# Kernel tuning notes

Measured on AMD Instinct MI355X. Metric: run time of the kernel, lower is better.

The kernel has to match this reference:

```python
import jax, jax.numpy as jnp
import numpy as np
from functools import partial

V, BS, L, H, C = 50257, 1024, 6, 12, 768
HD = C // H

def _ln(x, w, b):
    mu = jnp.mean(x, axis=-1, keepdims=True)
    var = jnp.var(x, axis=-1, keepdims=True)
    return (x - mu) * jax.lax.rsqrt(var + 1e-5) * w + b

def setup_inputs() -> dict:
    key = jax.random.key(0)
    ks = jax.random.split(key, 12)
    s = 0.02
    inp = {
        "idx": jax.random.randint(ks[0], (4, 1024), 0, V, dtype=jnp.int32),
        "wte": jax.random.normal(ks[1], (V, C), jnp.float32) * s,
        "wpe": jax.random.normal(ks[2], (BS, C), jnp.float32) * s,
        # per-block stacked params; linear weights stored [in, out]
        "ln1_w": jnp.ones((L, C)), "ln1_b": jnp.zeros((L, C)),
        "attn_w": jax.random.normal(ks[3], (L, C, 3 * C), jnp.float32) * s,
        "attn_b": jnp.zeros((L, 3 * C)),
        "proj_w": jax.random.normal(ks[4], (L, C, C), jnp.float32) * s,
        "proj_b": jnp.zeros((L, C)),
        "ln2_w": jnp.ones((L, C)), "ln2_b": jnp.zeros((L, C)),
        "fc_w": jax.random.normal(ks[5], (L, C, 4 * C), jnp.float32) * s,
        "fc_b": jnp.zeros((L, 4 * C)),
        "fc2_w": jax.random.normal(ks[6], (L, 4 * C, C), jnp.float32) * s,
        "fc2_b": jnp.zeros((L, C)),
        "lnf_w": jnp.ones((C,)), "lnf_b": jnp.zeros((C,)),
    }
    return inp

def _forward(idx, wte, wpe, ln1_w, ln1_b, attn_w, attn_b, proj_w, proj_b,
             ln2_w, ln2_b, fc_w, fc_b, fc2_w, fc2_b, lnf_w, lnf_b):
    B, T = idx.shape
    x = wte[idx] + wpe[:T]  # [B,T,C]
    causal = jnp.tril(jnp.ones((T, T), bool))  # [T,T]
    scale = 1.0 / np.sqrt(HD)
    neg_inf = jnp.finfo(x.dtype).min

    def block(x, p):
        l1w, l1b, aw, ab, pw, pb, l2w, l2b, fw, fb, f2w, f2b = p
        h = _ln(x, l1w, l1b)
        qkv = h @ aw + ab  # [B,T,3C]
        q, k, v = jnp.split(qkv, 3, axis=-1)
        q = q.reshape(B, T, H, HD)
        k = k.reshape(B, T, H, HD)
        v = v.reshape(B, T, H, HD)
        att = jnp.einsum('bqhd,bkhd->bhqk', q, k) * scale
        att = jnp.where(causal, att, neg_inf)
        att = jax.nn.softmax(att, axis=-1)
        y = jnp.einsum('bhqk,bkhd->bqhd', att, v).reshape(B, T, C)
        x = x + y @ pw + pb
        h = _ln(x, l2w, l2b)
        h = jax.nn.gelu(h @ fw + fb, approximate=False)  # torch nn.GELU default = exact
        x = x + h @ f2w + f2b
        return x, None

    params = (ln1_w, ln1_b, attn_w, attn_b, proj_w, proj_b,
              ln2_w, ln2_b, fc_w, fc_b, fc2_w, fc2_b)
    x, _ = jax.lax.scan(block, x, params)
    x = _ln(x, lnf_w, lnf_b)
    logits = x @ wte.T  # tied lm_head, no bias
    return logits

def reference(idx, wte, wpe, ln1_w, ln1_b, attn_w, attn_b, proj_w, proj_b,
              ln2_w, ln2_b, fc_w, fc_b, fc2_w, fc2_b, lnf_w, lnf_b):
    return _forward(idx, wte, wpe, ln1_w, ln1_b, attn_w, attn_b, proj_w, proj_b,
                    ln2_w, ln2_b, fc_w, fc_b, fc2_w, fc2_b, lnf_w, lnf_b)
```

## Files before the change

kernel.cpp:

```cpp
#include <hip/hip_runtime.h>

#define BT     4096
#define CDIM   768
#define NLAYER 6
#define NHEAD  12
#define VREAL  50257
#define VPAD   50432

typedef __bf16 bf16x8 __attribute__((ext_vector_type(8)));
typedef float  f32x4  __attribute__((ext_vector_type(4)));

__device__ __forceinline__ unsigned short f2bf(float f) {
    unsigned int u = __builtin_bit_cast(unsigned int, f);
    u += 0x7fffu + ((u >> 16) & 1u);
    return (unsigned short)(u >> 16);
}

__device__ __forceinline__ void gload16(const unsigned short* g, unsigned short* l) {
    __builtin_amdgcn_global_load_lds(
        (const __attribute__((address_space(1))) unsigned int*)g,
        (__attribute__((address_space(3))) unsigned int*)l, 16, 0, 0);
}

__device__ __forceinline__ void swz_block(int &bx, int &by) {
    int gx = gridDim.x;
    int nwg = gx * gridDim.y;
    if ((nwg & 7) == 0) {
        int lin = by * gx + bx;
        int q = nwg >> 3;
        lin = (lin & 7) * q + (lin >> 3);
        bx = lin % gx;
        by = lin / gx;
    }
}

__global__ __launch_bounds__(256) void transpose_conv(
    const float* __restrict__ in, unsigned short* __restrict__ out, int K, int N)
{
    in  += (size_t)blockIdx.z * K * N;
    out += (size_t)blockIdx.z * K * N;
    __shared__ float t[32][33];
    int j0 = blockIdx.x * 32;
    int i0 = blockIdx.y * 32;
    int c = threadIdx.x;
    int r = threadIdx.y;
    #pragma unroll
    for (int rr = r; rr < 32; rr += 8)
        t[rr][c] = in[(size_t)(i0 + rr) * N + j0 + c];
    __syncthreads();
    #pragma unroll
    for (int rr = r; rr < 32; rr += 8)
        out[(size_t)(j0 + rr) * K + i0 + c] = f2bf(t[c][rr]);
}

__global__ __launch_bounds__(256) void wteconv(
    const float* __restrict__ wte, unsigned short* __restrict__ out)
{
    size_t e = ((size_t)blockIdx.x * 256 + threadIdx.x) * 4;
    int row = (int)(e / CDIM);
    int col = (int)(e % CDIM);
    ushort4 o;
    if (row < VREAL) {
        float4 v = *(const float4*)(wte + (size_t)row * CDIM + col);
        o.x = f2bf(v.x); o.y = f2bf(v.y); o.z = f2bf(v.z); o.w = f2bf(v.w);
    } else {
        o.x = 0; o.y = 0; o.z = 0; o.w = 0;
    }
    *(ushort4*)(out + e) = o;
}

__global__ __launch_bounds__(256) void embed_kernel(
    const int* __restrict__ idx, const float* __restrict__ wte,
    const float* __restrict__ wpe, float* __restrict__ x)
{
    int row = blockIdx.x;
    int t = row & 1023;
    int id = idx[row];
    const float* s = wte + (size_t)id * CDIM;
    const float* p = wpe + (size_t)t * CDIM;
    float* o = x + (size_t)row * CDIM;
    for (int c = threadIdx.x; c < CDIM; c += 256) o[c] = s[c] + p[c];
}

__global__ __launch_bounds__(256) void ln_kernel(
    const float* __restrict__ x, const float* __restrict__ w,
    const float* __restrict__ b, unsigned short* __restrict__ out)
{
    int row = blockIdx.x * 4 + (threadIdx.x >> 6);
    int lane = threadIdx.x & 63;
    const float* xp = x + (size_t)row * CDIM;
    float4 v[3];
    float s = 0.f, sq = 0.f;
    #pragma unroll
    for (int j = 0; j < 3; ++j) {
        v[j] = *(const float4*)(xp + j * 256 + lane * 4);
        s  += v[j].x + v[j].y + v[j].z + v[j].w;
        sq += v[j].x * v[j].x + v[j].y * v[j].y
            + v[j].z * v[j].z + v[j].w * v[j].w;
    }
    #pragma unroll
    for (int o = 32; o > 0; o >>= 1) {
        s  += __shfl_xor(s, o, 64);
        sq += __shfl_xor(sq, o, 64);
    }
    float mu  = s * (1.f / CDIM);
    float var = sq * (1.f / CDIM) - mu * mu;
    float rs  = rsqrtf(var + 1e-5f);
    unsigned short* op = out + (size_t)row * CDIM;
    #pragma unroll
    for (int j = 0; j < 3; ++j) {
        int c = j * 256 + lane * 4;
        float4 w4 = *(const float4*)(w + c);
        float4 b4 = *(const float4*)(b + c);
        ushort4 o4;
        o4.x = f2bf((v[j].x - mu) * rs * w4.x + b4.x);
        o4.y = f2bf((v[j].y - mu) * rs * w4.y + b4.y);
        o4.z = f2bf((v[j].z - mu) * rs * w4.z + b4.z);
        o4.w = f2bf((v[j].w - mu) * rs * w4.w + b4.w);
        *(ushort4*)(op + c) = o4;
    }
}

template<int MODE>
__global__ __launch_bounds__(256) void gemm_kernel(
    const unsigned short* __restrict__ A, const unsigned short* __restrict__ Bt,
    const float* __restrict__ bias, const float* __restrict__ resid,
    float* __restrict__ outF, unsigned short* __restrict__ outB,
    unsigned short* __restrict__ qout, unsigned short* __restrict__ kout,
    unsigned short* __restrict__ vtout,
    int K, int Nout)
{
    __shared__ alignas(16) unsigned short As[2][4096];
    __shared__ alignas(16) unsigned short Bs[2][4096];
    const int tid  = threadIdx.x;
    const int wv   = tid >> 6;
    const int lane = tid & 63;
    const int m0 = blockIdx.x * 128;
    const int n0 = blockIdx.y * 128;
    const int wr = wv >> 1, wc = wv & 1;
    const int srow = lane >> 2;
    const int skk  = (lane & 3) * 8;
    const int fr = lane & 15;
    const int fg = lane >> 4;
    const int fk = fg * 8;

    f32x4 acc[4][4];
    #pragma unroll
    for (int i = 0; i < 4; ++i)
        #pragma unroll
        for (int j = 0; j < 4; ++j) acc[i][j] = f32x4{0.f, 0.f, 0.f, 0.f};

    for (int k0 = 0; k0 < K; k0 += 64) {
        #pragma unroll
        for (int j = 0; j < 2; ++j) {
            int row = j * 64 + wv * 16 + srow;
            const unsigned short* ga = A  + (size_t)(m0 + row) * K + k0 + skk;
            const unsigned short* gb = Bt + (size_t)(n0 + row) * K + k0 + skk;
            gload16(ga,      &As[0][j * 2048 + wv * 512]);
            gload16(ga + 32, &As[1][j * 2048 + wv * 512]);
            gload16(gb,      &Bs[0][j * 2048 + wv * 512]);
            gload16(gb + 32, &Bs[1][j * 2048 + wv * 512]);
        }
        __syncthreads();
        #pragma unroll
        for (int ks = 0; ks < 2; ++ks) {
            bf16x8 a[4], bb[4];
            #pragma unroll
            for (int m = 0; m < 4; ++m)
                a[m] = *(const bf16x8*)&As[ks][(wr * 64 + m * 16 + fr) * 32 + fk];
            #pragma unroll
            for (int n = 0; n < 4; ++n)
                bb[n] = *(const bf16x8*)&Bs[ks][(wc * 64 + n * 16 + fr) * 32 + fk];
            #pragma unroll
            for (int m = 0; m < 4; ++m)
                #pragma unroll
                for (int n = 0; n < 4; ++n)
                    acc[m][n] = __builtin_amdgcn_mfma_f32_16x16x32_bf16(
                        bb[n], a[m], acc[m][n], 0, 0, 0);
        }
        __syncthreads();
    }

    #pragma unroll
    for (int m = 0; m < 4; ++m) {
        int row = m0 + wr * 64 + m * 16 + fr;
        #pragma unroll
        for (int n = 0; n < 4; ++n) {
            int col = n0 + wc * 64 + n * 16 + fg * 4;
            float4 bs = *(const float4*)&bias[col];
            float u0 = acc[m][n][0] + bs.x;
            float u1 = acc[m][n][1] + bs.y;
            float u2 = acc[m][n][2] + bs.z;
            float u3 = acc[m][n][3] + bs.w;
            if (MODE == 2) {
                ushort4 p;
                p.x = f2bf(0.5f * u0 * (1.f + erff(u0 * 0.70710678118654752f)));
                p.y = f2bf(0.5f * u1 * (1.f + erff(u1 * 0.70710678118654752f)));
                p.z = f2bf(0.5f * u2 * (1.f + erff(u2 * 0.70710678118654752f)));
                p.w = f2bf(0.5f * u3 * (1.f + erff(u3 * 0.70710678118654752f)));
                *(ushort4*)&outB[(size_t)row * Nout + col] = p;
            } else if (MODE == 4) {
                int which = col / 768;
                int hh = (col - which * 768) >> 6;
                int dd = col & 63;
                int bb2 = row >> 10, tt = row & 1023;
                ushort4 v;
                v.x = f2bf(u0); v.y = f2bf(u1); v.z = f2bf(u2); v.w = f2bf(u3);
                if (which == 0)
                    *(ushort4*)&qout[(((size_t)bb2 * NHEAD + hh) * 1024 + tt) * 64 + dd] = v;
                else if (which == 1)
                    *(ushort4*)&kout[(((size_t)bb2 * NHEAD + hh) * 1024 + tt) * 64 + dd] = v;
                else {
                    vtout[(((size_t)bb2 * NHEAD + hh) * 64 + dd + 0) * 1024 + tt] = v.x;
                    vtout[(((size_t)bb2 * NHEAD + hh) * 64 + dd + 1) * 1024 + tt] = v.y;
                    vtout[(((size_t)bb2 * NHEAD + hh) * 64 + dd + 2) * 1024 + tt] = v.z;
                    vtout[(((size_t)bb2 * NHEAD + hh) * 64 + dd + 3) * 1024 + tt] = v.w;
                }
            }
        }
    }
}

__global__ __launch_bounds__(256) void gemm64_kernel(
    const unsigned short* __restrict__ A, const unsigned short* __restrict__ Bt,
    const float* __restrict__ bias, const float* __restrict__ resid,
    float* __restrict__ outF, int K, int Nout)
{
    __shared__ alignas(16) unsigned short As[2][2048];
    __shared__ alignas(16) unsigned short Bs[2][2048];
    const int tid  = threadIdx.x;
    const int wv   = tid >> 6;
    const int lane = tid & 63;
    const int m0 = blockIdx.x * 64;
    const int n0 = blockIdx.y * 64;
    const int wr = wv >> 1, wc = wv & 1;
    const int srow = lane >> 2;
    const int skk  = (lane & 3) * 8;
    const int fr = lane & 15;
    const int fg = lane >> 4;
    const int fk = fg * 8;

    f32x4 acc[2][2];
    #pragma unroll
    for (int i = 0; i < 2; ++i)
        #pragma unroll
        for (int j = 0; j < 2; ++j) acc[i][j] = f32x4{0.f, 0.f, 0.f, 0.f};

    for (int k0 = 0; k0 < K; k0 += 64) {
        int row = wv * 16 + srow;
        gload16(A  + (size_t)(m0 + row) * K + k0 + skk,      &As[0][wv * 512]);
        gload16(A  + (size_t)(m0 + row) * K + k0 + 32 + skk, &As[1][wv * 512]);
        gload16(Bt + (size_t)(n0 + row) * K + k0 + skk,      &Bs[0][wv * 512]);
        gload16(Bt + (size_t)(n0 + row) * K + k0 + 32 + skk, &Bs[1][wv * 512]);
        __syncthreads();
        #pragma unroll
        for (int ks = 0; ks < 2; ++ks) {
            bf16x8 a[2], bb[2];
            #pragma unroll
            for (int m = 0; m < 2; ++m)
                a[m] = *(const bf16x8*)&As[ks][(wr * 32 + m * 16 + fr) * 32 + fk];
            #pragma unroll
            for (int n = 0; n < 2; ++n)
                bb[n] = *(const bf16x8*)&Bs[ks][(wc * 32 + n * 16 + fr) * 32 + fk];
            #pragma unroll
            for (int m = 0; m < 2; ++m)
                #pragma unroll
                for (int n = 0; n < 2; ++n)
                    acc[m][n] = __builtin_amdgcn_mfma_f32_16x16x32_bf16(
                        bb[n], a[m], acc[m][n], 0, 0, 0);
        }
        __syncthreads();
    }

    #pragma unroll
    for (int m = 0; m < 2; ++m) {
        int row = m0 + wr * 32 + m * 16 + fr;
        #pragma unroll
        for (int n = 0; n < 2; ++n) {
            int col = n0 + wc * 32 + n * 16 + fg * 4;
            float4 rs = *(const float4*)&resid[(size_t)row * Nout + col];
            float4 bs = *(const float4*)&bias[col];
            float4 o;
            o.x = rs.x + acc[m][n][0] + bs.x;
            o.y = rs.y + acc[m][n][1] + bs.y;
            o.z = rs.z + acc[m][n][2] + bs.z;
            o.w = rs.w + acc[m][n][3] + bs.w;
            *(float4*)&outF[(size_t)row * Nout + col] = o;
        }
    }
}

__global__ __launch_bounds__(256, 2) void lmhead_kernel(
    const unsigned short* __restrict__ A, const unsigned short* __restrict__ Bt,
    float* __restrict__ outF)
{
    __shared__ alignas(16) unsigned short ldsA[3][8192];
    const int tid  = threadIdx.x;
    const int wv   = tid >> 6;
    const int lane = tid & 63;
    const int fr = lane & 15, fg = lane >> 4;
    int bx = blockIdx.x, by = blockIdx.y;
    swz_block(bx, by);
    const int m0 = blockIdx.z * 2048 + bx * 128;
    const int n0 = by * 256;

    const int srow = wv * 8 + (lane >> 3);
    const int sks  = ((lane & 7) * 8) ^ ((lane >> 3) << 3);

    const unsigned short* Bw = Bt + (size_t)(n0 + wv * 64 + fr) * 768 + fg * 8;

    const int swz0 = (fg * 8) ^ ((fr & 7) << 3);
    const int swz1 = (32 + fg * 8) ^ ((fr & 7) << 3);

    f32x4 acc[8][4];
    #pragma unroll
    for (int m = 0; m < 8; ++m)
        #pragma unroll
        for (int n = 0; n < 4; ++n) acc[m][n] = f32x4{0.f, 0.f, 0.f, 0.f};

    bf16x8 brE[4][2], brO[4][2];

#define LM_STAGE_A(t, buf)                                                    \
    {                                                                         \
        const int k0_ = (t) * 64;                                             \
        _Pragma("unroll")                                                     \
        for (int j = 0; j < 4; ++j)                                           \
            gload16(A + (size_t)(m0 + j * 32 + srow) * 768 + k0_ + sks,       \
                    &ldsA[buf][j * 2048 + wv * 512]);                         \
    }
#define LM_LOAD_B(t, br)                                                      \
    {                                                                         \
        const int k0_ = (t) * 64;                                             \
        _Pragma("unroll")                                                     \
        for (int nf = 0; nf < 4; ++nf) {                                      \
            br[nf][0] = *(const bf16x8*)(Bw + (size_t)nf * 16 * 768 + k0_);   \
            br[nf][1] = *(const bf16x8*)(Bw + (size_t)nf * 16 * 768 + k0_ + 32); \
        }                                                                     \
    }
#define LM_COMPUTE(buf, br)                                                   \
    {                                                                         \
        _Pragma("unroll")                                                     \
        for (int m = 0; m < 8; ++m) {                                         \
            bf16x8 a0 = *(const bf16x8*)&ldsA[buf][(m * 16 + fr) * 64 + swz0];\
            bf16x8 a1 = *(const bf16x8*)&ldsA[buf][(m * 16 + fr) * 64 + swz1];\
            _Pragma("unroll")                                                 \
            for (int nf = 0; nf < 4; ++nf) {                                  \
                acc[m][nf] = __builtin_amdgcn_mfma_f32_16x16x32_bf16(a0, br[nf][0], acc[m][nf], 0, 0, 0); \
                acc[m][nf] = __builtin_amdgcn_mfma_f32_16x16x32_bf16(a1, br[nf][1], acc[m][nf], 0, 0, 0); \
            }                                                                 \
        }                                                                     \
    }
#define LM_TILE(t, bufC, brC, bufN, brN)                                      \
    {                                                                         \
        LM_STAGE_A((t) + 1, bufN);                                            \
        LM_LOAD_B((t) + 1, brN);                                              \
        asm volatile("s_waitcnt vmcnt(12)" ::: "memory");                     \
        __builtin_amdgcn_s_barrier();                                         \
        __builtin_amdgcn_sched_barrier(0);                                    \
        __builtin_amdgcn_s_setprio(1);                                        \
        LM_COMPUTE(bufC, brC);                                                \
        __builtin_amdgcn_s_setprio(0);                                        \
    }
#define LM_TILE_LAST(bufC, brC)                                               \
    {                                                                         \
        asm volatile("s_waitcnt vmcnt(0)" ::: "memory");                      \
        __builtin_amdgcn_s_barrier();                                         \
        __builtin_amdgcn_sched_barrier(0);                                    \
        __builtin_amdgcn_s_setprio(1);                                        \
        LM_COMPUTE(bufC, brC);                                                \
        __builtin_amdgcn_s_setprio(0);                                        \
    }

    LM_STAGE_A(0, 0);
    LM_LOAD_B(0, brE);
    LM_TILE(0,  0, brE, 1, brO);
    LM_TILE(1,  1, brO, 2, brE);
    LM_TILE(2,  2, brE, 0, brO);
    LM_TILE(3,  0, brO, 1, brE);
    LM_TILE(4,  1, brE, 2, brO);
    LM_TILE(5,  2, brO, 0, brE);
    LM_TILE(6,  0, brE, 1, brO);
    LM_TILE(7,  1, brO, 2, brE);
    LM_TILE(8,  2, brE, 0, brO);
    LM_TILE(9,  0, brO, 1, brE);
    LM_TILE(10, 1, brE, 2, brO);
    LM_TILE_LAST(2, brO);
#undef LM_STAGE_A
#undef LM_LOAD_B
#undef LM_COMPUTE
#undef LM_TILE
#undef LM_TILE_LAST

    const int colb = n0 + wv * 64 + fr;
    const int rowb = m0 + fg * 4;
    #pragma unroll
    for (int m = 0; m < 8; ++m) {
        #pragma unroll
        for (int n = 0; n < 4; ++n) {
            int col = colb + n * 16;
            if (col < VREAL) {
                #pragma unroll
                for (int r = 0; r < 4; ++r) {
                    int row = rowb + m * 16 + r;
                    outF[(size_t)row * VREAL + col] = acc[m][n][r];
                }
            }
        }
    }
}

__global__ __launch_bounds__(256) void attn_mfma_kernel(
    const unsigned short* __restrict__ qb, const unsigned short* __restrict__ kb,
    const unsigned short* __restrict__ vtb, unsigned short* __restrict__ y)
{
    __shared__ alignas(16) unsigned short Ps[4][16][72];
    const int qt = 15 - blockIdx.x;
    const int h = blockIdx.y, b = blockIdx.z;
    const int w = threadIdx.x >> 6, lane = threadIdx.x & 63;
    const int fr = lane & 15;
    const int fg = lane >> 4;
    const size_t bh = (size_t)(b * NHEAD + h);
    const unsigned short* Qb = qb  + bh * 1024 * 64;
    const unsigned short* Kb = kb  + bh * 1024 * 64;
    const unsigned short* Vt = vtb + bh * 64 * 1024;
    const int q0 = qt * 64 + w * 16;

    bf16x8 aq[2];
    aq[0] = *(const bf16x8*)(Qb + (size_t)(q0 + fr) * 64 + fg * 8);
    aq[1] = *(const bf16x8*)(Qb + (size_t)(q0 + fr) * 64 + 32 + fg * 8);

    f32x4 o[4];
    #pragma unroll
    for (int c = 0; c < 4; ++c) o[c] = f32x4{0.f, 0.f, 0.f, 0.f};
    float m[4], l[4];
    #pragma unroll
    for (int r = 0; r < 4; ++r) { m[r] = -1e30f; l[r] = 0.f; }

    for (int kt = 0; kt <= qt; ++kt) {
        const unsigned short* Kt = Kb + (size_t)kt * 64 * 64;
        f32x4 s[4];
        #pragma unroll
        for (int c = 0; c < 4; ++c) {
            bf16x8 bk0 = *(const bf16x8*)(Kt + (size_t)(c * 16 + fr) * 64 + fg * 8);
            bf16x8 bk1 = *(const bf16x8*)(Kt + (size_t)(c * 16 + fr) * 64 + 32 + fg * 8);
            s[c] = f32x4{0.f, 0.f, 0.f, 0.f};
            s[c] = __builtin_amdgcn_mfma_f32_16x16x32_bf16(aq[0], bk0, s[c], 0, 0, 0);
            s[c] = __builtin_amdgcn_mfma_f32_16x16x32_bf16(aq[1], bk1, s[c], 0, 0, 0);
        }
        float sc[4][4];
        #pragma unroll
        for (int c = 0; c < 4; ++c)
            #pragma unroll
            for (int r = 0; r < 4; ++r) {
                float v = s[c][r] * 0.125f;
                if (kt == qt && (kt * 64 + c * 16 + fr) > (q0 + fg * 4 + r))
                    v = -1e30f;
                sc[c][r] = v;
            }
        #pragma unroll
        for (int r = 0; r < 4; ++r) {
            float tm = fmaxf(fmaxf(sc[0][r], sc[1][r]), fmaxf(sc[2][r], sc[3][r]));
            tm = fmaxf(tm, __shfl_xor(tm, 1, 64));
            tm = fmaxf(tm, __shfl_xor(tm, 2, 64));
            tm = fmaxf(tm, __shfl_xor(tm, 4, 64));
            tm = fmaxf(tm, __shfl_xor(tm, 8, 64));
            if (tm > m[r]) {
                float corr = __expf(m[r] - tm);
                m[r] = tm;
                l[r] *= corr;
                #pragma unroll
                for (int c = 0; c < 4; ++c) o[c][r] *= corr;
            }
            float ps = 0.f;
            #pragma unroll
            for (int c = 0; c < 4; ++c) {
                float p = __expf(sc[c][r] - m[r]);
                sc[c][r] = p;
                ps += p;
            }
            ps += __shfl_xor(ps, 1, 64);
            ps += __shfl_xor(ps, 2, 64);
            ps += __shfl_xor(ps, 4, 64);
            ps += __shfl_xor(ps, 8, 64);
            l[r] += ps;
            #pragma unroll
            for (int c = 0; c < 4; ++c)
                Ps[w][fg * 4 + r][c * 16 + fr] = f2bf(sc[c][r]);
        }
        asm volatile("s_waitcnt lgkmcnt(0)" ::: "memory");
        bf16x8 ap0 = *(const bf16x8*)&Ps[w][fr][fg * 8];
        bf16x8 ap1 = *(const bf16x8*)&Ps[w][fr][32 + fg * 8];
        #pragma unroll
        for (int c = 0; c < 4; ++c) {
            const unsigned short* vb = Vt + (size_t)(c * 16 + fr) * 1024 + kt * 64;
            bf16x8 bv0 = *(const bf16x8*)(vb + fg * 8);
            bf16x8 bv1 = *(const bf16x8*)(vb + 32 + fg * 8);
            o[c] = __builtin_amdgcn_mfma_f32_16x16x32_bf16(ap0, bv0, o[c], 0, 0, 0);
            o[c] = __builtin_amdgcn_mfma_f32_16x16x32_bf16(ap1, bv1, o[c], 0, 0, 0);
        }
        asm volatile("s_waitcnt lgkmcnt(0)" ::: "memory");
    }

    float inv[4];
    #pragma unroll
    for (int r = 0; r < 4; ++r) inv[r] = 1.f / l[r];
    #pragma unroll
    for (int c = 0; c < 4; ++c)
        #pragma unroll
        for (int r = 0; r < 4; ++r) {
            int q = q0 + fg * 4 + r;
            y[((size_t)(b * 1024 + q)) * CDIM + h * 64 + c * 16 + fr] =
                f2bf(o[c][r] * inv[r]);
        }
}

extern "C" void kernel_launch(void* const* d_in, const int* in_sizes, int n_in,
                              void* d_out, int out_size, void* d_ws, size_t ws_size,
                              hipStream_t stream) {
    (void)in_sizes; (void)n_in; (void)out_size; (void)ws_size;
    const int*   idx   = (const int*)  d_in[0];
    const float* wte   = (const float*)d_in[1];
    const float* wpe   = (const float*)d_in[2];
    const float* ln1w  = (const float*)d_in[3];
    const float* ln1b  = (const float*)d_in[4];
    const float* attnw = (const float*)d_in[5];
    const float* attnb = (const float*)d_in[6];
    const float* projw = (const float*)d_in[7];
    const float* projb = (const float*)d_in[8];
    const float* ln2w  = (const float*)d_in[9];
    const float* ln2b  = (const float*)d_in[10];
    const float* fcw   = (const float*)d_in[11];
    const float* fcb   = (const float*)d_in[12];
    const float* fc2w  = (const float*)d_in[13];
    const float* fc2b  = (const float*)d_in[14];
    const float* lnfw  = (const float*)d_in[15];
    const float* lnfb  = (const float*)d_in[16];
    float* out = (float*)d_out;

    char* ws = (char*)d_ws;
    size_t off = 0;
    auto alloc = [&](size_t bytes) {
        void* p = ws + off;
        off += (bytes + 255) & ~(size_t)255;
        return p;
    };
    float*          x      = (float*)         alloc((size_t)BT * CDIM * 4);
    unsigned short* hbuf   = (unsigned short*)alloc((size_t)BT * CDIM * 2);
    unsigned short* qbuf   = (unsigned short*)alloc((size_t)BT * CDIM * 2);
    unsigned short* kbuf   = (unsigned short*)alloc((size_t)BT * CDIM * 2);
    unsigned short* vtbuf  = (unsigned short*)alloc((size_t)BT * CDIM * 2);
    unsigned short* ybuf   = (unsigned short*)alloc((size_t)BT * CDIM * 2);
    unsigned short* fcact  = (unsigned short*)alloc((size_t)BT * 4 * CDIM * 2);
    unsigned short* wqkvT  = (unsigned short*)alloc((size_t)NLAYER * 3 * CDIM * CDIM * 2);
    unsigned short* wprojT = (unsigned short*)alloc((size_t)NLAYER * CDIM * CDIM * 2);
    unsigned short* wfcT   = (unsigned short*)alloc((size_t)NLAYER * 4 * CDIM * CDIM * 2);
    unsigned short* wfc2T  = (unsigned short*)alloc((size_t)NLAYER * 4 * CDIM * CDIM * 2);
    unsigned short* wteB   = (unsigned short*)alloc((size_t)VPAD * CDIM * 2);

    transpose_conv<<<dim3(3*CDIM/32,   CDIM/32, NLAYER), dim3(32,8), 0, stream>>>(attnw, wqkvT, CDIM, 3*CDIM);
    transpose_conv<<<dim3(  CDIM/32,   CDIM/32, NLAYER), dim3(32,8), 0, stream>>>(projw, wprojT, CDIM, CDIM);
    transpose_conv<<<dim3(4*CDIM/32,   CDIM/32, NLAYER), dim3(32,8), 0, stream>>>(fcw,  wfcT,  CDIM, 4*CDIM);
    transpose_conv<<<dim3(  CDIM/32, 4*CDIM/32, NLAYER), dim3(32,8), 0, stream>>>(fc2w, wfc2T, 4*CDIM, CDIM);
    wteconv<<<(VPAD * CDIM / 4) / 256, 256, 0, stream>>>(wte, wteB);
    embed_kernel<<<BT, 256, 0, stream>>>(idx, wte, wpe, x);

    for (int l = 0; l < NLAYER; ++l) {
        ln_kernel<<<BT/4, 256, 0, stream>>>(x, ln1w + l*CDIM, ln1b + l*CDIM, hbuf);
        gemm_kernel<4><<<dim3(BT/128, 3*CDIM/128), 256, 0, stream>>>(
            hbuf, wqkvT + (size_t)l*3*CDIM*CDIM, attnb + (size_t)l*3*CDIM,
            nullptr, nullptr, nullptr, qbuf, kbuf, vtbuf, CDIM, 3*CDIM);
        attn_mfma_kernel<<<dim3(16, NHEAD, 4), 256, 0, stream>>>(qbuf, kbuf, vtbuf, ybuf);
        gemm64_kernel<<<dim3(BT/64, CDIM/64), 256, 0, stream>>>(
            ybuf, wprojT + (size_t)l*CDIM*CDIM, projb + (size_t)l*CDIM,
            x, x, CDIM, CDIM);
        ln_kernel<<<BT/4, 256, 0, stream>>>(x, ln2w + l*CDIM, ln2b + l*CDIM, hbuf);
        gemm_kernel<2><<<dim3(BT/128, 4*CDIM/128), 256, 0, stream>>>(
            hbuf, wfcT + (size_t)l*4*CDIM*CDIM, fcb + (size_t)l*4*CDIM,
            nullptr, nullptr, fcact, nullptr, nullptr, nullptr, CDIM, 4*CDIM);
        gemm64_kernel<<<dim3(BT/64, CDIM/64), 256, 0, stream>>>(
            fcact, wfc2T + (size_t)l*4*CDIM*CDIM, fc2b + (size_t)l*CDIM,
            x, x, 4*CDIM, CDIM);
    }
    ln_kernel<<<BT/4, 256, 0, stream>>>(x, lnfw, lnfb, hbuf);
    lmhead_kernel<<<dim3(16, VPAD/256, 2), 256, 0, stream>>>(hbuf, wteB, out);
}
```

Baseline: 2.055 ms.

## Load B operand directly into registers with double-buffered prefetch in gemm64

Removes the LDS staging buffer for the B matrix in the 64x64 GEMM. Each wave now reads its B fragments straight from global memory into registers, ping-ponging between two register sets so the next K-step's B load overlaps the current MFMAs. A is still staged through LDS. This saves LDS traffic and shared memory, but it issues uncoalesced per-lane global loads, raises register pressure, and assumes K is a multiple of 128.

```diff
diff --git a/kernel.cpp b/kernel.cpp
--- a/kernel.cpp
+++ b/kernel.cpp
@@ -227,7 +227,6 @@
     float* __restrict__ outF, int K, int Nout)
 {
     __shared__ alignas(16) unsigned short As[2][2048];
-    __shared__ alignas(16) unsigned short Bs[2][2048];
     const int tid  = threadIdx.x;
     const int wv   = tid >> 6;
     const int lane = tid & 63;
@@ -240,37 +239,64 @@
     const int fg = lane >> 4;
     const int fk = fg * 8;
 
+    const unsigned short* Bw = Bt + (size_t)(n0 + wc * 32 + fr) * K + fg * 8;
+
     f32x4 acc[2][2];
     #pragma unroll
     for (int i = 0; i < 2; ++i)
         #pragma unroll
         for (int j = 0; j < 2; ++j) acc[i][j] = f32x4{0.f, 0.f, 0.f, 0.f};
 
-    for (int k0 = 0; k0 < K; k0 += 64) {
-        int row = wv * 16 + srow;
-        gload16(A  + (size_t)(m0 + row) * K + k0 + skk,      &As[0][wv * 512]);
-        gload16(A  + (size_t)(m0 + row) * K + k0 + 32 + skk, &As[1][wv * 512]);
-        gload16(Bt + (size_t)(n0 + row) * K + k0 + skk,      &Bs[0][wv * 512]);
-        gload16(Bt + (size_t)(n0 + row) * K + k0 + 32 + skk, &Bs[1][wv * 512]);
+    bf16x8 brE[2][2], brO[2][2];
+
+#define G64_STAGE_A(k0_)                                                      \
+    {                                                                         \
+        int row = wv * 16 + srow;                                             \
+        gload16(A + (size_t)(m0 + row) * K + (k0_) + skk,      &As[0][wv * 512]); \
+        gload16(A + (size_t)(m0 + row) * K + (k0_) + 32 + skk, &As[1][wv * 512]); \
+    }
+#define G64_LOAD_B(k0_, br)                                                   \
+    {                                                                         \
+        _Pragma("unroll")                                                     \
+        for (int n = 0; n < 2; ++n) {                                         \
+            br[n][0] = *(const bf16x8*)(Bw + (size_t)(n * 16) * K + (k0_));   \
+            br[n][1] = *(const bf16x8*)(Bw + (size_t)(n * 16) * K + (k0_) + 32); \
+        }                                                                     \
+    }
+#define G64_COMPUTE(br)                                                       \
+    {                                                                         \
+        _Pragma("unroll")                                                     \
+        for (int ks = 0; ks < 2; ++ks) {                                      \
+            bf16x8 a[2];                                                      \
+            _Pragma("unroll")                                                 \
+            for (int m = 0; m < 2; ++m)                                       \
+                a[m] = *(const bf16x8*)&As[ks][(wr * 32 + m * 16 + fr) * 32 + fk]; \
+            _Pragma("unroll")                                                 \
+            for (int m = 0; m < 2; ++m)                                       \
+                _Pragma("unroll")                                             \
+                for (int n = 0; n < 2; ++n)                                   \
+                    acc[m][n] = __builtin_amdgcn_mfma_f32_16x16x32_bf16(      \
+                        br[n][ks], a[m], acc[m][n], 0, 0, 0);                 \
+        }                                                                     \
+    }
+
+    G64_LOAD_B(0, brE);
+    #pragma unroll 1
+    for (int k0 = 0; k0 < K; k0 += 128) {
+        G64_STAGE_A(k0);
         __syncthreads();
-        #pragma unroll
-        for (int ks = 0; ks < 2; ++ks) {
-            bf16x8 a[2], bb[2];
-            #pragma unroll
-            for (int m = 0; m < 2; ++m)
-                a[m] = *(const bf16x8*)&As[ks][(wr * 32 + m * 16 + fr) * 32 + fk];
-            #pragma unroll
-            for (int n = 0; n < 2; ++n)
-                bb[n] = *(const bf16x8*)&Bs[ks][(wc * 32 + n * 16 + fr) * 32 + fk];
-            #pragma unroll
-            for (int m = 0; m < 2; ++m)
-                #pragma unroll
-                for (int n = 0; n < 2; ++n)
-                    acc[m][n] = __builtin_amdgcn_mfma_f32_16x16x32_bf16(
-                        bb[n], a[m], acc[m][n], 0, 0, 0);
-        }
+        G64_LOAD_B(k0 + 64, brO);
+        G64_COMPUTE(brE);
         __syncthreads();
-    }
+        G64_STAGE_A(k0 + 64);
+        __syncthreads();
+        if (k0 + 128 < K) G64_LOAD_B(k0 + 128, brE);
+        G64_COMPUTE(brO);
+        __syncthreads();
+    }
+#undef G64_STAGE_A
+#undef G64_LOAD_B
+#undef G64_COMPUTE
 
     #pragma unroll
     for (int m = 0; m < 2; ++m) {
```

New measurement: 2.286 ms. 11.3% more time.
